# Performance work log

Hardware: AMD Instinct MI355X
Metric: run time of the kernel (lower is better)

Reference implementation:

```python
import jax, jax.numpy as jnp
import numpy as np

EMBED_DIM = 1024
NUM_HEADS = 16
HEAD_DIM = EMBED_DIM // NUM_HEADS


def setup_inputs() -> dict:
    key = jax.random.key(0)
    ks = jax.random.split(key, 9)
    B, T, C = 2, 2048, EMBED_DIM
    s = 1.0 / np.sqrt(C)
    inp = {
        "x": jax.random.normal(ks[0], (B, T, C), dtype=jnp.float32),
        "Wq": jax.random.uniform(ks[1], (C, C), jnp.float32, -s, s),
        "bq": jax.random.uniform(ks[2], (C,), jnp.float32, -s, s),
        "Wk": jax.random.uniform(ks[3], (C, C), jnp.float32, -s, s),
        "bk": jax.random.uniform(ks[4], (C,), jnp.float32, -s, s),
        "Wv": jax.random.uniform(ks[5], (C, C), jnp.float32, -s, s),
        "bv": jax.random.uniform(ks[6], (C,), jnp.float32, -s, s),
        "Wo": jax.random.uniform(ks[7], (C, C), jnp.float32, -s, s),
        "bo": jax.random.uniform(ks[8], (C,), jnp.float32, -s, s),
    }
    return inp


def reference(x, Wq, bq, Wk, bk, Wv, bv, Wo, bo):
    B, T, C = x.shape
    H, D = NUM_HEADS, HEAD_DIM

    def heads(W, b):
        # [B,T,C] -> [B,H,T,D]
        return (x @ W + b).reshape(B, T, H, D).transpose(0, 2, 1, 3)

    q = heads(Wq, bq)
    k = heads(Wk, bk)
    v = heads(Wv, bv)

    scores = jnp.einsum('bhtd,bhsd->bhts', q, k) / np.sqrt(D).astype(np.float32)
    causal = jnp.tril(jnp.ones((T, T), dtype=bool))  # [T,T]
    scores = jnp.where(causal[None, None], scores, -jnp.inf)
    weights = jax.nn.softmax(scores, axis=-1)
    out = jnp.einsum('bhts,bhsd->bhtd', weights, v)  # [B,H,T,D]
    out = out.transpose(0, 2, 1, 3).reshape(B, T, C)
    return out @ Wo + bo
```

## Files before the change

kernel.cpp:

```cpp
#include <hip/hip_runtime.h>
#include <stdint.h>

#define T_LEN 2048
#define C_DIM 1024
#define NHEAD 16
#define HDIM  64
#define MTOT  4096

typedef __bf16 bf16;
typedef __bf16 bf16x4 __attribute__((ext_vector_type(4)));
typedef __bf16 bf16x8 __attribute__((ext_vector_type(8)));
typedef float  f32x4  __attribute__((ext_vector_type(4)));

__device__ __forceinline__ bf16 f2bf(float f) {
    union { float f; unsigned u; } x; x.f = f;
    unsigned r = x.u + 0x7fffu + ((x.u >> 16) & 1u);
    unsigned short h = (unsigned short)(r >> 16);
    return __builtin_bit_cast(bf16, h);
}

__device__ __forceinline__ void g2l16(const void* g, const void* l) {
    __builtin_amdgcn_global_load_lds(
        (const __attribute__((address_space(1))) unsigned int*)(uintptr_t)g,
        (__attribute__((address_space(3))) unsigned int*)(uint32_t)(uintptr_t)l,
        16, 0, 0);
}

__global__ void cast_xw_kernel(const float* __restrict__ x, bf16* __restrict__ xb,
                               const float* __restrict__ W0, const float* __restrict__ W1,
                               const float* __restrict__ W2, const float* __restrict__ W3,
                               bf16* __restrict__ wt) {
    __shared__ float tile[64][68];
    const int tid = threadIdx.x;
    const int bid = blockIdx.x;
    if (bid < 2048) {
        int f = bid * 256 + tid;
        const float4* p = (const float4*)x + (size_t)f * 2;
        float4 a = p[0], b = p[1];
        bf16x8 o;
        o[0] = f2bf(a.x); o[1] = f2bf(a.y); o[2] = f2bf(a.z); o[3] = f2bf(a.w);
        o[4] = f2bf(b.x); o[5] = f2bf(b.y); o[6] = f2bf(b.z); o[7] = f2bf(b.w);
        ((bf16x8*)xb)[f] = o;
        return;
    }
    const int i = bid - 2048;
    const int w = i >> 8;
    const int nt = (i >> 4) & 15;
    const int kt = i & 15;
    const float* W = (w == 0) ? W0 : (w == 1) ? W1 : (w == 2) ? W2 : W3;
    const int kb = kt * 64, nb = nt * 64;
#pragma unroll
    for (int pass = 0; pass < 4; ++pass) {
        int row = pass * 16 + (tid >> 4);
        int col = (tid & 15) * 4;
        float4 v = *(const float4*)(W + (size_t)(kb + row) * 1024 + nb + col);
        *(float4*)(&tile[row][col]) = v;
    }
    __syncthreads();
#pragma unroll
    for (int pass = 0; pass < 2; ++pass) {
        int s = pass * 256 + tid;
        int nn = s >> 3, c = s & 7;
        bf16x8 o;
#pragma unroll
        for (int j = 0; j < 8; ++j) o[j] = f2bf(tile[c * 8 + j][nn]);
        *(bf16x8*)(wt + (size_t)w * 1048576 + (size_t)(nb + nn) * 1024 + kb + c * 8) = o;
    }
}

__global__ void transpose_v_kernel(const bf16* __restrict__ V, bf16* __restrict__ Vtp) {
    __shared__ bf16 tile[128][72];
    const int tid = threadIdx.x;
    const int t0 = blockIdx.x * 128, bh = blockIdx.y;
    const size_t hb = (size_t)bh * 131072;
#pragma unroll
    for (int pass = 0; pass < 4; ++pass) {
        int s = pass * 256 + tid;
        int row = s >> 3, c = s & 7;
        bf16x8 v = *(const bf16x8*)(V + hb + (size_t)(t0 + row) * 64 + c * 8);
        *(bf16x8*)(&tile[row][c * 8]) = v;
    }
    __syncthreads();
#pragma unroll
    for (int pass = 0; pass < 4; ++pass) {
        int s = pass * 256 + tid;
        int d = s >> 4, ch = s & 15;
        bf16x8 o;
#pragma unroll
        for (int j = 0; j < 8; ++j) {
            int orig = 32 * (ch >> 2) + 16 * (j >> 2) + 4 * (ch & 3) + (j & 3);
            o[j] = tile[orig][d];
        }
        *(bf16x8*)(Vtp + hb + (size_t)d * 2048 + t0 + ch * 8) = o;
    }
}

__global__ __launch_bounds__(256, 2)
void gemm_qkv_kernel(const bf16* __restrict__ A, const bf16* __restrict__ Wt,
                     const float* __restrict__ b0, const float* __restrict__ b1,
                     const float* __restrict__ b2, bf16* __restrict__ outQKV) {
    __shared__ char lds[40960];
    bf16* As = (bf16*)lds;
    bf16* Bs = (bf16*)(lds + 16384);

    const int tid = threadIdx.x;
    const int lane = tid & 63, wid = tid >> 6;
    const int r = lane & 15, q4 = lane >> 4;
    const int mbase = blockIdx.y * 128;
    const int nbase = blockIdx.x * 192;
    const int wm = (wid >> 1) * 64;
    const int wn = (wid & 1) * 96;

    f32x4 acc[4][6];
#pragma unroll
    for (int i = 0; i < 4; ++i)
#pragma unroll
        for (int j = 0; j < 6; ++j) acc[i][j] = f32x4{0.f, 0.f, 0.f, 0.f};

    for (int kt = 0; kt < 16; ++kt) {
        int kb = kt * 64;
#pragma unroll
        for (int p = 0; p < 4; ++p) {
            int s = p * 256 + tid;
            int row = s >> 3, blk = s & 7;
            g2l16(A + (size_t)(mbase + row) * 1024 + kb + ((blk ^ (row & 7)) * 8), (char*)As + s * 16);
        }
#pragma unroll
        for (int p = 0; p < 6; ++p) {
            int s = p * 256 + tid;
            int row = s >> 3, blk = s & 7;
            g2l16(Wt + (size_t)(nbase + row) * 1024 + kb + ((blk ^ (row & 7)) * 8), (char*)Bs + s * 16);
        }
        __syncthreads();
#pragma unroll
        for (int ks = 0; ks < 2; ++ks) {
            int blk = ks * 4 + q4;
            bf16x8 a[4], b[6];
#pragma unroll
            for (int i = 0; i < 4; ++i) {
                int rowa = wm + i * 16 + r;
                a[i] = *(const bf16x8*)((const char*)As + rowa * 128 + ((blk ^ (rowa & 7)) * 16));
            }
#pragma unroll
            for (int j = 0; j < 6; ++j) {
                int rowb = wn + j * 16 + r;
                b[j] = *(const bf16x8*)((const char*)Bs + rowb * 128 + ((blk ^ (rowb & 7)) * 16));
            }
#pragma unroll
            for (int i = 0; i < 4; ++i)
#pragma unroll
                for (int j = 0; j < 6; ++j)
                    acc[i][j] = __builtin_amdgcn_mfma_f32_16x16x32_bf16(b[j], a[i], acc[i][j], 0, 0, 0);
        }
        __syncthreads();
    }

    const float QS = 0.18033688011112042f;
#pragma unroll
    for (int i = 0; i < 4; ++i) {
        int m = mbase + wm + i * 16 + r;
        int bi = m >> 11, t = m & 2047;
#pragma unroll
        for (int j = 0; j < 6; ++j) {
            int n0 = nbase + wn + j * 16 + q4 * 4;
            int z = n0 >> 10;
            int nz = n0 & 1023;
            const float* bias = (z == 0) ? b0 : (z == 1) ? b1 : b2;
            float4 bb = *(const float4*)(bias + nz);
            float osc = (z == 0) ? QS : 1.0f;
            bf16x4 w;
            w[0] = f2bf((acc[i][j][0] + bb.x) * osc);
            w[1] = f2bf((acc[i][j][1] + bb.y) * osc);
            w[2] = f2bf((acc[i][j][2] + bb.z) * osc);
            w[3] = f2bf((acc[i][j][3] + bb.w) * osc);
            int h = nz >> 6, d = nz & 63;
            *(bf16x4*)(outQKV + (size_t)z * 4194304 + ((size_t)(bi * 16 + h) * 2048 + t) * 64 + d) = w;
        }
    }
}

__global__ __launch_bounds__(256, 2)
void gemm_o_kernel(const bf16* __restrict__ A, const bf16* __restrict__ Bt,
                   const float* __restrict__ bias, float* __restrict__ out) {
    __shared__ char lds[24576];
    bf16* As = (bf16*)lds;
    bf16* Bs = (bf16*)(lds + 16384);

    const int tid = threadIdx.x;
    const int lane = tid & 63, wid = tid >> 6;
    const int r = lane & 15, q4 = lane >> 4;
    const int nb = blockIdx.x * 64;
    const int mb = blockIdx.y * 128;
    const int wm = (wid >> 1) * 64;
    const int wn = (wid & 1) * 32;

    float4 bvv[2];
#pragma unroll
    for (int j = 0; j < 2; ++j) bvv[j] = *(const float4*)(bias + nb + wn + j * 16 + q4 * 4);

    f32x4 acc[4][2];
#pragma unroll
    for (int i = 0; i < 4; ++i)
#pragma unroll
        for (int j = 0; j < 2; ++j) acc[i][j] = f32x4{0.f, 0.f, 0.f, 0.f};

    for (int kt = 0; kt < 16; ++kt) {
        int kb = kt * 64;
#pragma unroll
        for (int p = 0; p < 4; ++p) {
            int s = p * 256 + tid;
            int row = s >> 3, blk = s & 7;
            g2l16(A + (size_t)(mb + row) * 1024 + kb + ((blk ^ (row & 7)) * 8), (char*)As + s * 16);
        }
#pragma unroll
        for (int p = 0; p < 2; ++p) {
            int s = p * 256 + tid;
            int row = s >> 3, blk = s & 7;
            g2l16(Bt + (size_t)(nb + row) * 1024 + kb + ((blk ^ (row & 7)) * 8), (char*)Bs + s * 16);
        }
        __syncthreads();
#pragma unroll
        for (int ks = 0; ks < 2; ++ks) {
            int blk = ks * 4 + q4;
            bf16x8 a[4], b[2];
#pragma unroll
            for (int i = 0; i < 4; ++i) {
                int rowa = wm + i * 16 + r;
                a[i] = *(const bf16x8*)((const char*)As + rowa * 128 + ((blk ^ (rowa & 7)) * 16));
            }
#pragma unroll
            for (int j = 0; j < 2; ++j) {
                int rowb = wn + j * 16 + r;
                b[j] = *(const bf16x8*)((const char*)Bs + rowb * 128 + ((blk ^ (rowb & 7)) * 16));
            }
#pragma unroll
            for (int i = 0; i < 4; ++i)
#pragma unroll
                for (int j = 0; j < 2; ++j)
                    acc[i][j] = __builtin_amdgcn_mfma_f32_16x16x32_bf16(b[j], a[i], acc[i][j], 0, 0, 0);
        }
        __syncthreads();
    }

#pragma unroll
    for (int i = 0; i < 4; ++i) {
        int m = mb + wm + i * 16 + r;
#pragma unroll
        for (int j = 0; j < 2; ++j) {
            int n0 = nb + wn + j * 16 + q4 * 4;
            float4 w;
            w.x = acc[i][j][0] + bvv[j].x;
            w.y = acc[i][j][1] + bvv[j].y;
            w.z = acc[i][j][2] + bvv[j].z;
            w.w = acc[i][j][3] + bvv[j].w;
            *(float4*)(out + (size_t)m * 1024 + n0) = w;
        }
    }
}

__global__ __launch_bounds__(512, 2)
void attn_kernel(const bf16* __restrict__ Q, const bf16* __restrict__ K,
                 const bf16* __restrict__ Vtp, bf16* __restrict__ Aout) {
    __shared__ char lds[65536];

    const int tid = threadIdx.x, lane = tid & 63, wid = tid >> 6;
    const int r = lane & 15, q4 = lane >> 4;
    const int p = blockIdx.x >> 5;
    const int bh = blockIdx.x & 31;
    const int b = bh >> 4, h = bh & 15;
    const size_t hb = (size_t)bh * 131072;

    const int qi[2] = { p, 15 - p };
    const int ittot = 16 - p;

    bf16x8 qf[2][2];
#pragma unroll
    for (int i = 0; i < 2; ++i)
#pragma unroll
        for (int ks = 0; ks < 2; ++ks) {
            int row = qi[i] * 128 + wid * 16 + r;
            qf[i][ks] = *(const bf16x8*)(Q + hb + (size_t)row * 64 + ks * 32 + q4 * 8);
        }

    bf16x8 ones;
#pragma unroll
    for (int j = 0; j < 8; ++j) ones[j] = (bf16)1.0f;

    f32x4 o[2][4];
    f32x4 osum[2];
#pragma unroll
    for (int i = 0; i < 2; ++i) {
        osum[i] = f32x4{0.f, 0.f, 0.f, 0.f};
#pragma unroll
        for (int jd = 0; jd < 4; ++jd) o[i][jd] = f32x4{0.f, 0.f, 0.f, 0.f};
    }

    auto stage = [&](int buf, int kb) {
        char* Kb = lds + buf * 16384;
        char* Vb = lds + 32768 + buf * 16384;
#pragma unroll
        for (int pp = 0; pp < 2; ++pp) {
            int s = pp * 512 + tid;
            int row = s >> 3, blk = s & 7;
            g2l16(K + hb + (size_t)(kb + row) * 64 + ((blk ^ (row & 7)) * 8), Kb + s * 16);
        }
#pragma unroll
        for (int pp = 0; pp < 2; ++pp) {
            int s = pp * 512 + tid;
            int row = s >> 4, ch = s & 15;
            g2l16(Vtp + hb + (size_t)row * 2048 + kb + ((ch ^ (row & 15)) * 8), Vb + s * 16);
        }
    };

    stage(0, 0);

    for (int it = 0; it < ittot; ++it) {
        __syncthreads();
        const int cb = it & 1;
        if (it + 1 < ittot) stage((it + 1) & 1, (it + 1) * 128);
        const int kb = it * 128;
        const char* Kb = lds + cb * 16384;
        const char* Vb = lds + 32768 + cb * 16384;
        const bool aAct = (it <= qi[0]);

        f32x4 sc[2][8];
#pragma unroll
        for (int st = 0; st < 8; ++st) {
            int rowk = st * 16 + r;
            bf16x8 ak0 = *(const bf16x8*)(Kb + rowk * 128 + ((q4 ^ (rowk & 7)) * 16));
            bf16x8 ak1 = *(const bf16x8*)(Kb + rowk * 128 + (((4 + q4) ^ (rowk & 7)) * 16));
            sc[1][st] = __builtin_amdgcn_mfma_f32_16x16x32_bf16(ak0, qf[1][0], f32x4{0.f, 0.f, 0.f, 0.f}, 0, 0, 0);
            sc[1][st] = __builtin_amdgcn_mfma_f32_16x16x32_bf16(ak1, qf[1][1], sc[1][st], 0, 0, 0);
            if (aAct) {
                sc[0][st] = __builtin_amdgcn_mfma_f32_16x16x32_bf16(ak0, qf[0][0], f32x4{0.f, 0.f, 0.f, 0.f}, 0, 0, 0);
                sc[0][st] = __builtin_amdgcn_mfma_f32_16x16x32_bf16(ak1, qf[0][1], sc[0][st], 0, 0, 0);
            }
        }

#pragma unroll
        for (int i = 0; i < 2; ++i) {
            if (i == 0 && !aAct) continue;
            const bool dia = (it == qi[i]);
            int qrow = qi[i] * 128 + wid * 16 + r;
            bf16x8 pb[4];
#pragma unroll
            for (int c = 0; c < 4; ++c) {
                bf16x8 t;
                if (dia) {
#pragma unroll
                    for (int j = 0; j < 8; ++j) {
                        int st = 2 * c + (j >> 2), reg = j & 3;
                        int key = kb + st * 16 + q4 * 4 + reg;
                        float sv = (key > qrow) ? -1e30f : sc[i][st][reg];
                        t[j] = (bf16)__builtin_amdgcn_exp2f(sv);
                    }
                } else {
#pragma unroll
                    for (int j = 0; j < 8; ++j) {
                        int st = 2 * c + (j >> 2), reg = j & 3;
                        t[j] = (bf16)__builtin_amdgcn_exp2f(sc[i][st][reg]);
                    }
                }
                pb[c] = t;
            }
#pragma unroll
            for (int c = 0; c < 4; ++c) {
                int sidx = c * 4 + q4;
                osum[i] = __builtin_amdgcn_mfma_f32_16x16x32_bf16(ones, pb[c], osum[i], 0, 0, 0);
#pragma unroll
                for (int dsub = 0; dsub < 4; ++dsub) {
                    int rowd = dsub * 16 + r;
                    bf16x8 av = *(const bf16x8*)(Vb + rowd * 256 + ((sidx ^ (rowd & 15)) * 16));
                    o[i][dsub] = __builtin_amdgcn_mfma_f32_16x16x32_bf16(av, pb[c], o[i][dsub], 0, 0, 0);
                }
            }
        }
    }

#pragma unroll
    for (int i = 0; i < 2; ++i) {
        float inv = 1.f / osum[i][0];
        int q = qi[i] * 128 + wid * 16 + r;
#pragma unroll
        for (int dsub = 0; dsub < 4; ++dsub) {
            bf16x4 w;
#pragma unroll
            for (int reg = 0; reg < 4; ++reg) w[reg] = f2bf(o[i][dsub][reg] * inv);
            *(bf16x4*)(Aout + ((size_t)(b * 2048 + q)) * 1024 + h * 64 + dsub * 16 + q4 * 4) = w;
        }
    }
}


extern "C" void kernel_launch(void* const* d_in, const int* in_sizes, int n_in,
                              void* d_out, int out_size, void* d_ws, size_t ws_size,
                              hipStream_t stream) {
    const float* x  = (const float*)d_in[0];
    const float* Wq = (const float*)d_in[1];
    const float* bq = (const float*)d_in[2];
    const float* Wk = (const float*)d_in[3];
    const float* bk = (const float*)d_in[4];
    const float* Wv = (const float*)d_in[5];
    const float* bv = (const float*)d_in[6];
    const float* Wo = (const float*)d_in[7];
    const float* bo = (const float*)d_in[8];
    float* out = (float*)d_out;

    char* ws = (char*)d_ws;
    bf16* xb   = (bf16*)(ws);
    bf16* wt   = (bf16*)(ws + 8388608);
    bf16* qkv  = (bf16*)(ws + 16777216);
    bf16* vtp  = (bf16*)(ws + 41943040);
    bf16* attn = (bf16*)(ws + 50331648);

    hipLaunchKernelGGL(cast_xw_kernel, dim3(3072), dim3(256), 0, stream,
                       x, xb, Wq, Wk, Wv, Wo, wt);
    hipLaunchKernelGGL(gemm_qkv_kernel, dim3(16, 32), dim3(256), 0, stream,
                       xb, wt, bq, bk, bv, qkv);
    hipLaunchKernelGGL(transpose_v_kernel, dim3(16, 32), dim3(256), 0, stream,
                       qkv + (size_t)2 * 4194304, vtp);
    hipLaunchKernelGGL(attn_kernel, dim3(256), dim3(512), 0, stream,
                       qkv, qkv + 4194304, vtp, attn);
    hipLaunchKernelGGL(gemm_o_kernel, dim3(16, 32), dim3(256), 0, stream,
                       attn, wt + (size_t)3 * 1048576, bo, out);
}
```

Measured before the change: 171.1 us.

## Double-buffer GEMM LDS loads and split attention into per-query-tile blocks

Result: slower. 179.6 us (+4.9%).

```diff
diff --git a/kernel.cpp b/kernel.cpp
--- a/kernel.cpp
+++ b/kernel.cpp
@@ -100,8 +100,6 @@
                      const float* __restrict__ b0, const float* __restrict__ b1,
                      const float* __restrict__ b2, bf16* __restrict__ outQKV) {
     __shared__ char lds[40960];
-    bf16* As = (bf16*)lds;
-    bf16* Bs = (bf16*)(lds + 16384);
 
     const int tid = threadIdx.x;
     const int lane = tid & 63, wid = tid >> 6;
@@ -117,42 +115,50 @@
 #pragma unroll
         for (int j = 0; j < 6; ++j) acc[i][j] = f32x4{0.f, 0.f, 0.f, 0.f};
 
-    for (int kt = 0; kt < 16; ++kt) {
-        int kb = kt * 64;
-#pragma unroll
-        for (int p = 0; p < 4; ++p) {
+    auto stage = [&](int buf, int kb) {
+        char* As = lds + buf * 20480;
+        char* Bs = As + 8192;
+#pragma unroll
+        for (int p = 0; p < 2; ++p) {
             int s = p * 256 + tid;
-            int row = s >> 3, blk = s & 7;
-            g2l16(A + (size_t)(mbase + row) * 1024 + kb + ((blk ^ (row & 7)) * 8), (char*)As + s * 16);
-        }
-#pragma unroll
-        for (int p = 0; p < 6; ++p) {
+            int row = s >> 2, sl = s & 3;
+            int c = sl ^ ((row >> 1) & 3);
+            g2l16(A + (size_t)(mbase + row) * 1024 + kb + c * 8, As + s * 16);
+        }
+#pragma unroll
+        for (int p = 0; p < 3; ++p) {
             int s = p * 256 + tid;
-            int row = s >> 3, blk = s & 7;
-            g2l16(Wt + (size_t)(nbase + row) * 1024 + kb + ((blk ^ (row & 7)) * 8), (char*)Bs + s * 16);
-        }
+            int row = s >> 2, sl = s & 3;
+            int c = sl ^ ((row >> 1) & 3);
+            g2l16(Wt + (size_t)(nbase + row) * 1024 + kb + c * 8, Bs + s * 16);
+        }
+    };
+
+    stage(0, 0);
+
+    for (int kt = 0; kt < 32; ++kt) {
         __syncthreads();
-#pragma unroll
-        for (int ks = 0; ks < 2; ++ks) {
-            int blk = ks * 4 + q4;
-            bf16x8 a[4], b[6];
-#pragma unroll
-            for (int i = 0; i < 4; ++i) {
-                int rowa = wm + i * 16 + r;
-                a[i] = *(const bf16x8*)((const char*)As + rowa * 128 + ((blk ^ (rowa & 7)) * 16));
-            }
-#pragma unroll
-            for (int j = 0; j < 6; ++j) {
-                int rowb = wn + j * 16 + r;
-                b[j] = *(const bf16x8*)((const char*)Bs + rowb * 128 + ((blk ^ (rowb & 7)) * 16));
-            }
-#pragma unroll
-            for (int i = 0; i < 4; ++i)
-#pragma unroll
-                for (int j = 0; j < 6; ++j)
-                    acc[i][j] = __builtin_amdgcn_mfma_f32_16x16x32_bf16(b[j], a[i], acc[i][j], 0, 0, 0);
-        }
-        __syncthreads();
+        const int cb = kt & 1;
+        if (kt < 31) stage(cb ^ 1, (kt + 1) * 32);
+        const char* As = lds + cb * 20480;
+        const char* Bs = As + 8192;
+
+        bf16x8 a[4], b[6];
+#pragma unroll
+        for (int i = 0; i < 4; ++i) {
+            int rowa = wm + i * 16 + r;
+            a[i] = *(const bf16x8*)(As + rowa * 64 + ((q4 ^ ((rowa >> 1) & 3)) * 16));
+        }
+#pragma unroll
+        for (int j = 0; j < 6; ++j) {
+            int rowb = wn + j * 16 + r;
+            b[j] = *(const bf16x8*)(Bs + rowb * 64 + ((q4 ^ ((rowb >> 1) & 3)) * 16));
+        }
+#pragma unroll
+        for (int i = 0; i < 4; ++i)
+#pragma unroll
+            for (int j = 0; j < 6; ++j)
+                acc[i][j] = __builtin_amdgcn_mfma_f32_16x16x32_bf16(b[j], a[i], acc[i][j], 0, 0, 0);
     }
 
     const float QS = 0.18033688011112042f;
@@ -182,9 +188,7 @@
 __global__ __launch_bounds__(256, 2)
 void gemm_o_kernel(const bf16* __restrict__ A, const bf16* __restrict__ Bt,
                    const float* __restrict__ bias, float* __restrict__ out) {
-    __shared__ char lds[24576];
-    bf16* As = (bf16*)lds;
-    bf16* Bs = (bf16*)(lds + 16384);
+    __shared__ char lds[49152];
 
     const int tid = threadIdx.x;
     const int lane = tid & 63, wid = tid >> 6;
@@ -204,21 +208,31 @@
 #pragma unroll
         for (int j = 0; j < 2; ++j) acc[i][j] = f32x4{0.f, 0.f, 0.f, 0.f};
 
-    for (int kt = 0; kt < 16; ++kt) {
-        int kb = kt * 64;
+    auto stage = [&](int buf, int kb) {
+        char* As = lds + buf * 24576;
+        char* Bs = As + 16384;
 #pragma unroll
         for (int p = 0; p < 4; ++p) {
             int s = p * 256 + tid;
             int row = s >> 3, blk = s & 7;
-            g2l16(A + (size_t)(mb + row) * 1024 + kb + ((blk ^ (row & 7)) * 8), (char*)As + s * 16);
+            g2l16(A + (size_t)(mb + row) * 1024 + kb + ((blk ^ (row & 7)) * 8), As + s * 16);
         }
 #pragma unroll
         for (int p = 0; p < 2; ++p) {
             int s = p * 256 + tid;
             int row = s >> 3, blk = s & 7;
-            g2l16(Bt + (size_t)(nb + row) * 1024 + kb + ((blk ^ (row & 7)) * 8), (char*)Bs + s * 16);
-        }
+            g2l16(Bt + (size_t)(nb + row) * 1024 + kb + ((blk ^ (row & 7)) * 8), Bs + s * 16);
+        }
+    };
+
+    stage(0, 0);
+
+    for (int kt = 0; kt < 16; ++kt) {
         __syncthreads();
+        const int cb = kt & 1;
+        if (kt < 15) stage(cb ^ 1, (kt + 1) * 64);
+        const char* As = lds + cb * 24576;
+        const char* Bs = As + 16384;
 #pragma unroll
         for (int ks = 0; ks < 2; ++ks) {
             int blk = ks * 4 + q4;
@@ -226,12 +240,12 @@
 #pragma unroll
             for (int i = 0; i < 4; ++i) {
                 int rowa = wm + i * 16 + r;
-                a[i] = *(const bf16x8*)((const char*)As + rowa * 128 + ((blk ^ (rowa & 7)) * 16));
+                a[i] = *(const bf16x8*)(As + rowa * 128 + ((blk ^ (rowa & 7)) * 16));
             }
 #pragma unroll
             for (int j = 0; j < 2; ++j) {
                 int rowb = wn + j * 16 + r;
-                b[j] = *(const bf16x8*)((const char*)Bs + rowb * 128 + ((blk ^ (rowb & 7)) * 16));
+                b[j] = *(const bf16x8*)(Bs + rowb * 128 + ((blk ^ (rowb & 7)) * 16));
             }
 #pragma unroll
             for (int i = 0; i < 4; ++i)
@@ -239,7 +253,6 @@
                 for (int j = 0; j < 2; ++j)
                     acc[i][j] = __builtin_amdgcn_mfma_f32_16x16x32_bf16(b[j], a[i], acc[i][j], 0, 0, 0);
         }
-        __syncthreads();
     }
 
 #pragma unroll
@@ -258,27 +271,25 @@
     }
 }
 
-__global__ __launch_bounds__(512, 2)
+__global__ __launch_bounds__(256, 2)
 void attn_kernel(const bf16* __restrict__ Q, const bf16* __restrict__ K,
                  const bf16* __restrict__ Vtp, bf16* __restrict__ Aout) {
     __shared__ char lds[65536];
 
     const int tid = threadIdx.x, lane = tid & 63, wid = tid >> 6;
     const int r = lane & 15, q4 = lane >> 4;
-    const int p = blockIdx.x >> 5;
-    const int bh = blockIdx.x & 31;
+    const int id = blockIdx.x;
+    const int qi = (id < 256) ? (id >> 5) : (15 - ((id - 256) >> 5));
+    const int bh = id & 31;
     const int b = bh >> 4, h = bh & 15;
     const size_t hb = (size_t)bh * 131072;
 
-    const int qi[2] = { p, 15 - p };
-    const int ittot = 16 - p;
-
     bf16x8 qf[2][2];
 #pragma unroll
     for (int i = 0; i < 2; ++i)
 #pragma unroll
         for (int ks = 0; ks < 2; ++ks) {
-            int row = qi[i] * 128 + wid * 16 + r;
+            int row = qi * 128 + wid * 32 + i * 16 + r;
             qf[i][ks] = *(const bf16x8*)(Q + hb + (size_t)row * 64 + ks * 32 + q4 * 8);
         }
 
@@ -296,17 +307,17 @@
     }
 
     auto stage = [&](int buf, int kb) {
-        char* Kb = lds + buf * 16384;
-        char* Vb = lds + 32768 + buf * 16384;
-#pragma unroll
-        for (int pp = 0; pp < 2; ++pp) {
-            int s = pp * 512 + tid;
+        char* Kb = lds + buf * 32768;
+        char* Vb = Kb + 16384;
+#pragma unroll
+        for (int pp = 0; pp < 4; ++pp) {
+            int s = pp * 256 + tid;
             int row = s >> 3, blk = s & 7;
             g2l16(K + hb + (size_t)(kb + row) * 64 + ((blk ^ (row & 7)) * 8), Kb + s * 16);
         }
 #pragma unroll
-        for (int pp = 0; pp < 2; ++pp) {
-            int s = pp * 512 + tid;
+        for (int pp = 0; pp < 4; ++pp) {
+            int s = pp * 256 + tid;
             int row = s >> 4, ch = s & 15;
             g2l16(Vtp + hb + (size_t)row * 2048 + kb + ((ch ^ (row & 15)) * 8), Vb + s * 16);
         }
@@ -314,14 +325,13 @@
 
     stage(0, 0);
 
-    for (int it = 0; it < ittot; ++it) {
+    for (int kt = 0; kt <= qi; ++kt) {
         __syncthreads();
-        const int cb = it & 1;
-        if (it + 1 < ittot) stage((it + 1) & 1, (it + 1) * 128);
-        const int kb = it * 128;
-        const char* Kb = lds + cb * 16384;
-        const char* Vb = lds + 32768 + cb * 16384;
-        const bool aAct = (it <= qi[0]);
+        const int cb = kt & 1;
+        if (kt < qi) stage(cb ^ 1, (kt + 1) * 128);
+        const int kb = kt * 128;
+        const char* Kb = lds + cb * 32768;
+        const char* Vb = Kb + 16384;
 
         f32x4 sc[2][8];
 #pragma unroll
@@ -329,20 +339,18 @@
             int rowk = st * 16 + r;
             bf16x8 ak0 = *(const bf16x8*)(Kb + rowk * 128 + ((q4 ^ (rowk & 7)) * 16));
             bf16x8 ak1 = *(const bf16x8*)(Kb + rowk * 128 + (((4 + q4) ^ (rowk & 7)) * 16));
-            sc[1][st] = __builtin_amdgcn_mfma_f32_16x16x32_bf16(ak0, qf[1][0], f32x4{0.f, 0.f, 0.f, 0.f}, 0, 0, 0);
-            sc[1][st] = __builtin_amdgcn_mfma_f32_16x16x32_bf16(ak1, qf[1][1], sc[1][st], 0, 0, 0);
-            if (aAct) {
-                sc[0][st] = __builtin_amdgcn_mfma_f32_16x16x32_bf16(ak0, qf[0][0], f32x4{0.f, 0.f, 0.f, 0.f}, 0, 0, 0);
-                sc[0][st] = __builtin_amdgcn_mfma_f32_16x16x32_bf16(ak1, qf[0][1], sc[0][st], 0, 0, 0);
+#pragma unroll
+            for (int i = 0; i < 2; ++i) {
+                sc[i][st] = __builtin_amdgcn_mfma_f32_16x16x32_bf16(ak0, qf[i][0], f32x4{0.f, 0.f, 0.f, 0.f}, 0, 0, 0);
+                sc[i][st] = __builtin_amdgcn_mfma_f32_16x16x32_bf16(ak1, qf[i][1], sc[i][st], 0, 0, 0);
             }
         }
 
+        const bool dia = (kt == qi);
+        bf16x8 pb[2][4];
 #pragma unroll
         for (int i = 0; i < 2; ++i) {
-            if (i == 0 && !aAct) continue;
-            const bool dia = (it == qi[i]);
-            int qrow = qi[i] * 128 + wid * 16 + r;
-            bf16x8 pb[4];
+            int qrow = qi * 128 + wid * 32 + i * 16 + r;
 #pragma unroll
             for (int c = 0; c < 4; ++c) {
                 bf16x8 t;
@@ -361,18 +369,21 @@
                         t[j] = (bf16)__builtin_amdgcn_exp2f(sc[i][st][reg]);
                     }
                 }
-                pb[c] = t;
+                pb[i][c] = t;
             }
-#pragma unroll
-            for (int c = 0; c < 4; ++c) {
-                int sidx = c * 4 + q4;
-                osum[i] = __builtin_amdgcn_mfma_f32_16x16x32_bf16(ones, pb[c], osum[i], 0, 0, 0);
-#pragma unroll
-                for (int dsub = 0; dsub < 4; ++dsub) {
-                    int rowd = dsub * 16 + r;
-                    bf16x8 av = *(const bf16x8*)(Vb + rowd * 256 + ((sidx ^ (rowd & 15)) * 16));
-                    o[i][dsub] = __builtin_amdgcn_mfma_f32_16x16x32_bf16(av, pb[c], o[i][dsub], 0, 0, 0);
-                }
+        }
+
+#pragma unroll
+        for (int c = 0; c < 4; ++c) {
+            int sidx = c * 4 + q4;
+            osum[0] = __builtin_amdgcn_mfma_f32_16x16x32_bf16(ones, pb[0][c], osum[0], 0, 0, 0);
+            osum[1] = __builtin_amdgcn_mfma_f32_16x16x32_bf16(ones, pb[1][c], osum[1], 0, 0, 0);
+#pragma unroll
+            for (int dsub = 0; dsub < 4; ++dsub) {
+                int rowd = dsub * 16 + r;
+                bf16x8 av = *(const bf16x8*)(Vb + rowd * 256 + ((sidx ^ (rowd & 15)) * 16));
+                o[0][dsub] = __builtin_amdgcn_mfma_f32_16x16x32_bf16(av, pb[0][c], o[0][dsub], 0, 0, 0);
+                o[1][dsub] = __builtin_amdgcn_mfma_f32_16x16x32_bf16(av, pb[1][c], o[1][dsub], 0, 0, 0);
             }
         }
     }
@@ -380,7 +391,7 @@
 #pragma unroll
     for (int i = 0; i < 2; ++i) {
         float inv = 1.f / osum[i][0];
-        int q = qi[i] * 128 + wid * 16 + r;
+        int q = qi * 128 + wid * 32 + i * 16 + r;
 #pragma unroll
         for (int dsub = 0; dsub < 4; ++dsub) {
             bf16x4 w;
@@ -419,7 +430,7 @@
                        xb, wt, bq, bk, bv, qkv);
     hipLaunchKernelGGL(transpose_v_kernel, dim3(16, 32), dim3(256), 0, stream,
                        qkv + (size_t)2 * 4194304, vtp);
-    hipLaunchKernelGGL(attn_kernel, dim3(256), dim3(512), 0, stream,
+    hipLaunchKernelGGL(attn_kernel, dim3(512), dim3(256), 0, stream,
                        qkv, qkv + 4194304, vtp, attn);
     hipLaunchKernelGGL(gemm_o_kernel, dim3(16, 32), dim3(256), 0, stream,
                        attn, wt + (size_t)3 * 1048576, bo, out);
```
